# Performance work log

Hardware: AMD Instinct MI355X
Metric: run time of the kernel (lower is better)

## Reference

```python
import jax, jax.numpy as jnp
import numpy as np

INPUT_SIZE = 3072
CORE_SIZE = 1024
OUTPUT_SIZE = 100
BATCH = 8192


def _ri(key, shape, lo, hi):
    # small-range int8 values (torch rand*scale cast to int8)
    return jax.random.randint(key, shape, lo, hi, dtype=jnp.int32).astype(jnp.int8)


def setup_inputs() -> dict:
    key = jax.random.key(0)
    ks = jax.random.split(key, 14)
    return {
        # learned int8 weights (nonzero after EQI.apply updates)
        "W_itoc": _ri(ks[0], (INPUT_SIZE, CORE_SIZE), -3, 4),
        "W_itoc_b": _ri(ks[1], (CORE_SIZE,), -3, 4),
        "W_ctoc": _ri(ks[2], (CORE_SIZE, CORE_SIZE), -3, 4),
        "W_ctoc_b": _ri(ks[3], (CORE_SIZE,), -3, 4),
        "W_ctoo": _ri(ks[4], (CORE_SIZE, OUTPUT_SIZE), -3, 4),
        "W_ctoo_b": _ri(ks[5], (OUTPUT_SIZE,), -3, 4),
        # epsilon perturbations: EPSILON_SCALE=2 -> values in {-1,0,1}
        "e_itoc": _ri(ks[6], (INPUT_SIZE, CORE_SIZE), -2, 2),
        "e_itoc_b": _ri(ks[7], (CORE_SIZE,), -2, 2),
        "e_ctoc": _ri(ks[8], (CORE_SIZE, CORE_SIZE), -2, 2),
        "e_ctoc_b": _ri(ks[9], (CORE_SIZE,), -2, 2),
        "e_ctoo": _ri(ks[10], (CORE_SIZE, OUTPUT_SIZE), -2, 2),
        "e_ctoo_b": _ri(ks[11], (OUTPUT_SIZE,), -2, 2),
        # forward activations
        "inputs": _ri(ks[12], (BATCH, INPUT_SIZE), -4, 5),
        "hiddens": _ri(ks[13], (BATCH, CORE_SIZE), -4, 5),
    }


def _addmm_i8(x, w, b):
    # int8 addmm with wraparound semantics: accumulate in int32, cast back
    # to int8 (truncation == mod-256, matching torch int8 arithmetic).
    acc = jnp.matmul(x.astype(jnp.int32), w.astype(jnp.int32)) + b.astype(jnp.int32)
    return acc.astype(jnp.int8)


def reference(W_itoc, W_itoc_b, W_ctoc, W_ctoc_b, W_ctoo, W_ctoo_b,
              e_itoc, e_itoc_b, e_ctoc, e_ctoc_b, e_ctoo, e_ctoo_b,
              inputs, hiddens):
    # layer 1: inputs -> core (weight = W + epsilon, elementwise int8 add)
    i2c = _addmm_i8(inputs, W_itoc + e_itoc, W_itoc_b + e_itoc_b)      # [B, CORE]
    # layer 2: (hiddens + projected inputs) -> core
    h2 = _addmm_i8(hiddens + i2c, W_ctoc + e_ctoc, W_ctoc_b + e_ctoc_b)  # [B, CORE]
    # layer 3: core -> output
    out = _addmm_i8(h2, W_ctoo + e_ctoo, W_ctoo_b + e_ctoo_b)          # [B, OUT]
    return (h2, out)
```

## Files before the change

### kernel.cpp

```cpp
#include <hip/hip_runtime.h>

typedef int v4i  __attribute__((ext_vector_type(4)));
typedef int v16i __attribute__((ext_vector_type(16)));

__device__ __forceinline__ int pack4i(int a, int b, int c, int d) {
  return (a & 255) | ((b & 255) << 8) | ((c & 255) << 16) | ((d & 255) << 24);
}
__device__ __forceinline__ int badd4(int a, int b) {
  return ((a & 0x7f7f7f7f) + (b & 0x7f7f7f7f)) ^ ((a ^ b) & 0x80808080);
}

__device__ void pack_tile(const int* __restrict__ W, const int* __restrict__ E,
                          char* __restrict__ Bt, int K, int N,
                          int nx, int ky, char* lin) {
  const int t = threadIdx.x;
  const int n0 = nx * 64, k0 = ky * 256;
  {
    const int kk = t >> 2, c = t & 3;
    for (int p = 0; p < 4; ++p) {
      const int k = kk + (p << 6);
      const long grow = (long)(k0 + k) * N;
      #pragma unroll
      for (int i = 0; i < 4; ++i) {
        const int nl = (c << 4) + (i << 2);
        const int ng = n0 + nl;
        int a0, a1, a2, a3;
        if (ng + 3 < N) {
          int4 wv = *(const int4*)(W + grow + ng);
          int4 ev = *(const int4*)(E + grow + ng);
          a0 = wv.x + ev.x; a1 = wv.y + ev.y; a2 = wv.z + ev.z; a3 = wv.w + ev.w;
        } else {
          a0 = (ng + 0 < N) ? W[grow + ng + 0] + E[grow + ng + 0] : 0;
          a1 = (ng + 1 < N) ? W[grow + ng + 1] + E[grow + ng + 1] : 0;
          a2 = (ng + 2 < N) ? W[grow + ng + 2] + E[grow + ng + 2] : 0;
          a3 = (ng + 3 < N) ? W[grow + ng + 3] + E[grow + ng + 3] : 0;
        }
        *(int*)(lin + k * 68 + nl) = pack4i(a0, a1, a2, a3);
      }
    }
  }
  __syncthreads();
  {
    const int n = t & 63, kq = t >> 6;
    char* dst = Bt + (long)(n0 + n) * K + k0 + (kq << 6);
    int outv[16];
    #pragma unroll
    for (int g = 0; g < 16; ++g) {
      const int k = (kq << 6) + (g << 2);
      outv[g] = pack4i(lin[(k + 0) * 68 + n], lin[(k + 1) * 68 + n],
                       lin[(k + 2) * 68 + n], lin[(k + 3) * 68 + n]);
    }
    #pragma unroll
    for (int g = 0; g < 4; ++g)
      *(int4*)(dst + (g << 4)) =
          make_int4(outv[g * 4], outv[g * 4 + 1], outv[g * 4 + 2], outv[g * 4 + 3]);
  }
}

__device__ void pack_i32_to_i8(const int* __restrict__ src, char* __restrict__ dst,
                               long base, int iters) {
  const int t = threadIdx.x;
  for (int i = 0; i < iters; ++i) {
    const long i0 = base + ((long)(t + i * 256) << 4);
    const int* s = src + i0;
    int4 v0 = *(const int4*)(s);
    int4 v1 = *(const int4*)(s + 4);
    int4 v2 = *(const int4*)(s + 8);
    int4 v3 = *(const int4*)(s + 12);
    *(int4*)(dst + i0) = make_int4(
        pack4i(v0.x, v0.y, v0.z, v0.w), pack4i(v1.x, v1.y, v1.z, v1.w),
        pack4i(v2.x, v2.y, v2.z, v2.w), pack4i(v3.x, v3.y, v3.z, v3.w));
  }
}

__global__ __launch_bounds__(256) void pack_all_kernel(
    const int* W1, const int* E1, char* Bt1,
    const int* W2, const int* E2, char* Bt2,
    const int* W3, const int* E3, char* Bt3,
    const int* b1, const int* eb1, int* bs1,
    const int* b2, const int* eb2, int* bs2,
    const int* b3, const int* eb3, int* bs3,
    const int* X, char* X8, const int* H, char* H8) {
  __shared__ __align__(16) char lin[256 * 68];
  const int bid = blockIdx.x;
  if (bid < 192) {
    pack_tile(W1, E1, Bt1, 3072, 1024, bid % 16, bid / 16, lin);
  } else if (bid < 256) {
    const int l = bid - 192;
    pack_tile(W2, E2, Bt2, 1024, 1024, l % 16, l / 16, lin);
  } else if (bid < 264) {
    const int l = bid - 256;
    pack_tile(W3, E3, Bt3, 1024, 100, l & 1, l >> 1, lin);
  } else if (bid == 264) {
    const int t = threadIdx.x;
    for (int i = t; i < 1024; i += 256) {
      bs1[i] = b1[i] + eb1[i];
      bs2[i] = b2[i] + eb2[i];
    }
    for (int i = t; i < 128; i += 256)
      bs3[i] = (i < 100) ? (b3[i] + eb3[i]) : 0;
  } else if (bid < 1289) {
    pack_i32_to_i8(X, X8, (long)(bid - 265) * 24576, 6);
  } else {
    pack_i32_to_i8(H, H8, (long)(bid - 1289) * 32768, 8);
  }
}

template<int EPI>
__global__ __launch_bounds__(256, 4) void gemm_kernel(
    const char* __restrict__ A, const char* __restrict__ Btg,
    const int* __restrict__ bsum, const char* __restrict__ H8,
    char* __restrict__ A8out, int* __restrict__ Iout, const int K) {
  __shared__ __align__(16) char smem[30720];

  const int t = threadIdx.x;
  const int bid = blockIdx.x;
  const int mt = bid & 127, nt = bid >> 7;
  const long m0 = (long)mt << 6;
  const int n0 = nt << 7;

  const int lane = t & 63, w = t >> 6;
  const int lc = lane & 31, hg = lane >> 5;

  v16i acc[2] = {};

  const int am = t >> 2, ah = t & 3;
  const char* Arow = A + (m0 + am) * (long)K + ah * 16;
  const int aoff = am * 80 + ah * 16;
  const int bm = t >> 1, bh = t & 1;
  const char* Brow = Btg + (long)(n0 + bm) * K + bh * 32;
  const int boff = bm * 80 + bh * 32;

  const int abo = lc * 80 + hg * 16;
  const int bbo = (w * 32 + lc) * 80 + hg * 16;

  int4 ar, br0, br1;
  auto LOAD = [&](int kb) {
    ar  = *(const int4*)(Arow + kb);
    br0 = *(const int4*)(Brow + kb);
    br1 = *(const int4*)(Brow + kb + 16);
  };
  auto STORE = [&](int stage) {
    char* base = smem + stage * 15360;
    *(int4*)(base + aoff) = ar;
    *(int4*)(base + 5120 + boff)      = br0;
    *(int4*)(base + 5120 + boff + 16) = br1;
  };

  const int kiters = K >> 6;
  LOAD(0);
  STORE(0);
  __syncthreads();

  for (int kt = 0; kt < kiters; ++kt) {
    if (kt + 1 < kiters) LOAD((kt + 1) << 6);
    const char* base = smem + (kt & 1) * 15360;
    const char* Ab = base + abo;
    const char* Bb = base + 5120 + bbo;
    #pragma unroll
    for (int ks = 0; ks < 2; ++ks) {
      v4i a0 = *(const v4i*)(Ab + ks * 32);
      v4i a1 = *(const v4i*)(Ab + 32 * 80 + ks * 32);
      v4i b  = *(const v4i*)(Bb + ks * 32);
      acc[0] = __builtin_amdgcn_mfma_i32_32x32x32_i8(a0, b, acc[0], 0, 0, 0);
      acc[1] = __builtin_amdgcn_mfma_i32_32x32x32_i8(a1, b, acc[1], 0, 0, 0);
    }
    if (kt + 1 < kiters) {
      STORE((kt + 1) & 1);
      __syncthreads();
    }
  }

  const int gcl = w * 32 + lc;
  const int bs = bsum[n0 + gcl];
  if (EPI == 1) {
    #pragma unroll
    for (int tm = 0; tm < 2; ++tm) {
      #pragma unroll
      for (int r = 0; r < 16; ++r) {
        const int row = tm * 32 + (hg << 2) + (r & 3) + ((r >> 2) << 3);
        Iout[(m0 + row) * 1024 + n0 + gcl] = (int)(signed char)(acc[tm][r] + bs);
      }
    }
  } else {
    __syncthreads();
    #pragma unroll
    for (int tm = 0; tm < 2; ++tm) {
      #pragma unroll
      for (int r = 0; r < 16; ++r) {
        const int row = tm * 32 + (hg << 2) + (r & 3) + ((r >> 2) << 3);
        smem[row * 144 + gcl] = (char)(acc[tm][r] + bs);
      }
    }
    __syncthreads();
    const char* src = smem + (t >> 2) * 144 + (t & 3) * 32;
    const long gm = m0 + (t >> 2);
    const long gco = gm * 1024 + n0 + (t & 3) * 32;
    int4 s0 = *(const int4*)(src);
    int4 s1 = *(const int4*)(src + 16);
    int4 h0 = *(const int4*)(H8 + gco);
    int4 h1 = *(const int4*)(H8 + gco + 16);
    s0 = make_int4(badd4(s0.x, h0.x), badd4(s0.y, h0.y),
                   badd4(s0.z, h0.z), badd4(s0.w, h0.w));
    s1 = make_int4(badd4(s1.x, h1.x), badd4(s1.y, h1.y),
                   badd4(s1.z, h1.z), badd4(s1.w, h1.w));
    *(int4*)(A8out + gco)      = s0;
    *(int4*)(A8out + gco + 16) = s1;
  }
}

__global__ __launch_bounds__(256, 2) void gemm3_kernel(
    const int* __restrict__ h2, const char* __restrict__ Btg,
    const int* __restrict__ bsum, int* __restrict__ Iout) {
  __shared__ __align__(16) char smem[25600];
  const int t = threadIdx.x;
  const int m0 = blockIdx.x << 5;
  const int lane = t & 63, w = t >> 6;
  const int lc = lane & 31, hg = lane >> 5;
  v16i acc = {};

  const int am = t >> 3, ah = t & 7;
  const long arow = (long)(m0 + am) * 1024 + ah * 8;
  const int aoff = am * 80 + ah * 8;
  const int bm = t >> 1, bh = t & 1;
  const char* Brow = Btg + (long)bm * 1024 + bh * 32;
  const int boff = bm * 80 + bh * 32;

  int4 ar[2]; int4 br[2];
  auto LOAD = [&](int kb) {
    const int* Ar = h2 + arow + kb;
    ar[0] = *(const int4*)(Ar);
    ar[1] = *(const int4*)(Ar + 4);
    br[0] = *(const int4*)(Brow + kb);
    br[1] = *(const int4*)(Brow + kb + 16);
  };
  auto STORE = [&](int stage) {
    char* As_ = smem + stage * 12800;
    char* Bs_ = As_ + 2560;
    int2 d;
    d.x = pack4i(ar[0].x, ar[0].y, ar[0].z, ar[0].w);
    d.y = pack4i(ar[1].x, ar[1].y, ar[1].z, ar[1].w);
    *(int2*)(As_ + aoff) = d;
    *(int4*)(Bs_ + boff)      = br[0];
    *(int4*)(Bs_ + boff + 16) = br[1];
  };

  LOAD(0); STORE(0); __syncthreads();
  for (int kt = 0; kt < 16; ++kt) {
    if (kt + 1 < 16) LOAD((kt + 1) << 6);
    const char* base = smem + (kt & 1) * 12800;
    const char* Ab = base + lc * 80 + hg * 16;
    const char* Bb = base + 2560 + (w * 32 + lc) * 80 + hg * 16;
    #pragma unroll
    for (int ks = 0; ks < 2; ++ks) {
      v4i a = *(const v4i*)(Ab + ks * 32);
      v4i b = *(const v4i*)(Bb + ks * 32);
      acc = __builtin_amdgcn_mfma_i32_32x32x32_i8(a, b, acc, 0, 0, 0);
    }
    if (kt + 1 < 16) { STORE((kt + 1) & 1); __syncthreads(); }
  }

  const int gcl = w * 32 + lc;
  if (gcl < 100) {
    const int bs = bsum[gcl];
    #pragma unroll
    for (int r = 0; r < 16; ++r) {
      const int row = (r & 3) + ((r >> 2) << 3) + (hg << 2);
      Iout[(long)(m0 + row) * 100 + gcl] = (int)(signed char)(acc[r] + bs);
    }
  }
}

extern "C" void kernel_launch(void* const* d_in, const int* in_sizes, int n_in,
                              void* d_out, int out_size, void* d_ws, size_t ws_size,
                              hipStream_t stream) {
  (void)in_sizes; (void)n_in; (void)out_size; (void)ws_size;
  const int* W1  = (const int*)d_in[0];
  const int* b1  = (const int*)d_in[1];
  const int* W2  = (const int*)d_in[2];
  const int* b2  = (const int*)d_in[3];
  const int* W3  = (const int*)d_in[4];
  const int* b3  = (const int*)d_in[5];
  const int* E1  = (const int*)d_in[6];
  const int* eb1 = (const int*)d_in[7];
  const int* E2  = (const int*)d_in[8];
  const int* eb2 = (const int*)d_in[9];
  const int* E3  = (const int*)d_in[10];
  const int* eb3 = (const int*)d_in[11];
  const int* X   = (const int*)d_in[12];
  const int* H   = (const int*)d_in[13];
  int* out = (int*)d_out;

  char* ws  = (char*)d_ws;
  char* Bt1 = ws;
  char* Bt2 = Bt1 + 3145728;
  char* Bt3 = Bt2 + 1048576;
  int*  bs1 = (int*)(Bt3 + 131072);
  int*  bs2 = bs1 + 1024;
  int*  bs3 = bs2 + 1024;
  char* A2  = (char*)(bs3 + 128);
  char* X8  = (char*)d_out;
  char* H8  = X8 + 25165824;

  pack_all_kernel<<<dim3(1545), dim3(256), 0, stream>>>(
      W1, E1, Bt1, W2, E2, Bt2, W3, E3, Bt3,
      b1, eb1, bs1, b2, eb2, bs2, b3, eb3, bs3, X, X8, H, H8);

  gemm_kernel<0><<<dim3(1024), dim3(256), 0, stream>>>(
      X8, Bt1, bs1, H8, A2, nullptr, 3072);

  gemm_kernel<1><<<dim3(1024), dim3(256), 0, stream>>>(
      A2, Bt2, bs2, nullptr, nullptr, out, 1024);

  gemm3_kernel<<<dim3(256), dim3(256), 0, stream>>>(
      out, Bt3, bs3, out + 8388608);
}
```

Measured before the change: 315.2 us.

## Deepen register prefetch in GEMM loops and batch loads in int8 packing

The GEMM main loops are unrolled by two and now hold two register sets, so global loads for tiles k+2 and k+3 are issued while MFMAs run on the current shared-memory stage. This gives memory latency more time to hide behind compute. The int32-to-int8 packing routine now issues G groups of loads before doing any packing or stores, which raises memory-level parallelism. The cost is higher register pressure, which could lower occupancy under the launch bounds.

```diff
diff --git a/kernel.cpp b/kernel.cpp
--- a/kernel.cpp
+++ b/kernel.cpp
@@ -57,19 +57,30 @@
   }
 }
 
-__device__ void pack_i32_to_i8(const int* __restrict__ src, char* __restrict__ dst,
-                               long base, int iters) {
+template<int G>
+__device__ void pack_ilp(const int* __restrict__ src, char* __restrict__ dst,
+                         long base, int supers) {
   const int t = threadIdx.x;
-  for (int i = 0; i < iters; ++i) {
-    const long i0 = base + ((long)(t + i * 256) << 4);
-    const int* s = src + i0;
-    int4 v0 = *(const int4*)(s);
-    int4 v1 = *(const int4*)(s + 4);
-    int4 v2 = *(const int4*)(s + 8);
-    int4 v3 = *(const int4*)(s + 12);
-    *(int4*)(dst + i0) = make_int4(
-        pack4i(v0.x, v0.y, v0.z, v0.w), pack4i(v1.x, v1.y, v1.z, v1.w),
-        pack4i(v2.x, v2.y, v2.z, v2.w), pack4i(v3.x, v3.y, v3.z, v3.w));
+  for (int s = 0; s < supers; ++s) {
+    int4 v[G][4];
+    #pragma unroll
+    for (int g = 0; g < G; ++g) {
+      const long i0 = base + ((long)(t + (s * G + g) * 256) << 4);
+      const int* p = src + i0;
+      v[g][0] = ((const int4*)p)[0];
+      v[g][1] = ((const int4*)p)[1];
+      v[g][2] = ((const int4*)p)[2];
+      v[g][3] = ((const int4*)p)[3];
+    }
+    #pragma unroll
+    for (int g = 0; g < G; ++g) {
+      const long i0 = base + ((long)(t + (s * G + g) * 256) << 4);
+      *(int4*)(dst + i0) = make_int4(
+          pack4i(v[g][0].x, v[g][0].y, v[g][0].z, v[g][0].w),
+          pack4i(v[g][1].x, v[g][1].y, v[g][1].z, v[g][1].w),
+          pack4i(v[g][2].x, v[g][2].y, v[g][2].z, v[g][2].w),
+          pack4i(v[g][3].x, v[g][3].y, v[g][3].z, v[g][3].w));
+    }
   }
 }
 
@@ -100,9 +111,9 @@
     for (int i = t; i < 128; i += 256)
       bs3[i] = (i < 100) ? (b3[i] + eb3[i]) : 0;
   } else if (bid < 1289) {
-    pack_i32_to_i8(X, X8, (long)(bid - 265) * 24576, 6);
+    pack_ilp<3>(X, X8, (long)(bid - 265) * 24576, 2);
   } else {
-    pack_i32_to_i8(H, H8, (long)(bid - 1289) * 32768, 8);
+    pack_ilp<4>(H, H8, (long)(bid - 1289) * 32768, 2);
   }
 }
 
@@ -134,27 +145,22 @@
   const int abo = lc * 80 + hg * 16;
   const int bbo = (w * 32 + lc) * 80 + hg * 16;
 
-  int4 ar, br0, br1;
-  auto LOAD = [&](int kb) {
-    ar  = *(const int4*)(Arow + kb);
-    br0 = *(const int4*)(Brow + kb);
-    br1 = *(const int4*)(Brow + kb + 16);
-  };
-  auto STORE = [&](int stage) {
+  int4 a0r, b0r0, b0r1;
+  int4 a1r, b1r0, b1r1;
+
+  auto LOAD = [&](int kb, int4& a, int4& b0, int4& b1) {
+    a  = *(const int4*)(Arow + kb);
+    b0 = *(const int4*)(Brow + kb);
+    b1 = *(const int4*)(Brow + kb + 16);
+  };
+  auto STORE = [&](int stage, const int4& a, const int4& b0, const int4& b1) {
     char* base = smem + stage * 15360;
-    *(int4*)(base + aoff) = ar;
-    *(int4*)(base + 5120 + boff)      = br0;
-    *(int4*)(base + 5120 + boff + 16) = br1;
-  };
-
-  const int kiters = K >> 6;
-  LOAD(0);
-  STORE(0);
-  __syncthreads();
-
-  for (int kt = 0; kt < kiters; ++kt) {
-    if (kt + 1 < kiters) LOAD((kt + 1) << 6);
-    const char* base = smem + (kt & 1) * 15360;
+    *(int4*)(base + aoff) = a;
+    *(int4*)(base + 5120 + boff)      = b0;
+    *(int4*)(base + 5120 + boff + 16) = b1;
+  };
+  auto MFMA = [&](int stage) {
+    const char* base = smem + stage * 15360;
     const char* Ab = base + abo;
     const char* Bb = base + 5120 + bbo;
     #pragma unroll
@@ -165,8 +171,23 @@
       acc[0] = __builtin_amdgcn_mfma_i32_32x32x32_i8(a0, b, acc[0], 0, 0, 0);
       acc[1] = __builtin_amdgcn_mfma_i32_32x32x32_i8(a1, b, acc[1], 0, 0, 0);
     }
-    if (kt + 1 < kiters) {
-      STORE((kt + 1) & 1);
+  };
+
+  const int kiters = K >> 6;
+  LOAD(0, a0r, b0r0, b0r1);
+  STORE(0, a0r, b0r0, b0r1);
+  LOAD(64, a1r, b1r0, b1r1);
+  __syncthreads();
+
+  for (int kt = 0; kt < kiters; kt += 2) {
+    MFMA(0);
+    if (kt + 2 < kiters) LOAD((kt + 2) << 6, a0r, b0r0, b0r1);
+    STORE(1, a1r, b1r0, b1r1);
+    __syncthreads();
+    MFMA(1);
+    if (kt + 3 < kiters) LOAD((kt + 3) << 6, a1r, b1r0, b1r1);
+    if (kt + 2 < kiters) {
+      STORE(0, a0r, b0r0, b0r1);
       __syncthreads();
     }
   }
@@ -226,29 +247,29 @@
   const char* Brow = Btg + (long)bm * 1024 + bh * 32;
   const int boff = bm * 80 + bh * 32;
 
-  int4 ar[2]; int4 br[2];
-  auto LOAD = [&](int kb) {
+  int4 a0r0, a0r1, b0r0, b0r1;
+  int4 a1r0, a1r1, b1r0, b1r1;
+
+  auto LOAD = [&](int kb, int4& a0, int4& a1, int4& b0, int4& b1) {
     const int* Ar = h2 + arow + kb;
-    ar[0] = *(const int4*)(Ar);
-    ar[1] = *(const int4*)(Ar + 4);
-    br[0] = *(const int4*)(Brow + kb);
-    br[1] = *(const int4*)(Brow + kb + 16);
-  };
-  auto STORE = [&](int stage) {
+    a0 = *(const int4*)(Ar);
+    a1 = *(const int4*)(Ar + 4);
+    b0 = *(const int4*)(Brow + kb);
+    b1 = *(const int4*)(Brow + kb + 16);
+  };
+  auto STORE = [&](int stage, const int4& a0, const int4& a1,
+                   const int4& b0, const int4& b1) {
     char* As_ = smem + stage * 12800;
     char* Bs_ = As_ + 2560;
     int2 d;
-    d.x = pack4i(ar[0].x, ar[0].y, ar[0].z, ar[0].w);
-    d.y = pack4i(ar[1].x, ar[1].y, ar[1].z, ar[1].w);
+    d.x = pack4i(a0.x, a0.y, a0.z, a0.w);
+    d.y = pack4i(a1.x, a1.y, a1.z, a1.w);
     *(int2*)(As_ + aoff) = d;
-    *(int4*)(Bs_ + boff)      = br[0];
-    *(int4*)(Bs_ + boff + 16) = br[1];
-  };
-
-  LOAD(0); STORE(0); __syncthreads();
-  for (int kt = 0; kt < 16; ++kt) {
-    if (kt + 1 < 16) LOAD((kt + 1) << 6);
-    const char* base = smem + (kt & 1) * 12800;
+    *(int4*)(Bs_ + boff)      = b0;
+    *(int4*)(Bs_ + boff + 16) = b1;
+  };
+  auto MFMA = [&](int stage) {
+    const char* base = smem + stage * 12800;
     const char* Ab = base + lc * 80 + hg * 16;
     const char* Bb = base + 2560 + (w * 32 + lc) * 80 + hg * 16;
     #pragma unroll
@@ -257,7 +278,24 @@
       v4i b = *(const v4i*)(Bb + ks * 32);
       acc = __builtin_amdgcn_mfma_i32_32x32x32_i8(a, b, acc, 0, 0, 0);
     }
-    if (kt + 1 < 16) { STORE((kt + 1) & 1); __syncthreads(); }
+  };
+
+  LOAD(0, a0r0, a0r1, b0r0, b0r1);
+  STORE(0, a0r0, a0r1, b0r0, b0r1);
+  LOAD(64, a1r0, a1r1, b1r0, b1r1);
+  __syncthreads();
+
+  for (int kt = 0; kt < 16; kt += 2) {
+    MFMA(0);
+    if (kt + 2 < 16) LOAD((kt + 2) << 6, a0r0, a0r1, b0r0, b0r1);
+    STORE(1, a1r0, a1r1, b1r0, b1r1);
+    __syncthreads();
+    MFMA(1);
+    if (kt + 3 < 16) LOAD((kt + 3) << 6, a1r0, a1r1, b1r0, b1r1);
+    if (kt + 2 < 16) {
+      STORE(0, a0r0, a0r1, b0r0, b0r1);
+      __syncthreads();
+    }
   }
 
   const int gcl = w * 32 + lc;
```

Measured after the change: 321.7 us. 1.02x slower.

## Fuse int32-to-int8 activation packing into GEMM loads; retile final GEMM

Applied to the files above, without the earlier changes.

Drops the separate pass that converted the int32 X and H activations to int8. The first GEMM now reads int32 X directly and packs it to int8 when staging into shared memory, and its epilogue reads int32 H directly. This removes one write and one re-read of the int8 copies. In exchange, layer 1 reads its A operand as int32 on every N-tile block, which is 4x the bytes per load and repeated across the 8 N tiles. The third GEMM moves to 16x16x64 MFMA with 16-row tiles and twice as many blocks, to spread it across more compute units.

```diff
diff --git a/kernel.cpp b/kernel.cpp
--- a/kernel.cpp
+++ b/kernel.cpp
@@ -57,30 +57,13 @@
   }
 }
 
-__device__ void pack_i32_to_i8(const int* __restrict__ src, char* __restrict__ dst,
-                               long base, int iters) {
-  const int t = threadIdx.x;
-  for (int i = 0; i < iters; ++i) {
-    const long i0 = base + ((long)(t + i * 256) << 4);
-    const int* s = src + i0;
-    int4 v0 = *(const int4*)(s);
-    int4 v1 = *(const int4*)(s + 4);
-    int4 v2 = *(const int4*)(s + 8);
-    int4 v3 = *(const int4*)(s + 12);
-    *(int4*)(dst + i0) = make_int4(
-        pack4i(v0.x, v0.y, v0.z, v0.w), pack4i(v1.x, v1.y, v1.z, v1.w),
-        pack4i(v2.x, v2.y, v2.z, v2.w), pack4i(v3.x, v3.y, v3.z, v3.w));
-  }
-}
-
 __global__ __launch_bounds__(256) void pack_all_kernel(
     const int* W1, const int* E1, char* Bt1,
     const int* W2, const int* E2, char* Bt2,
     const int* W3, const int* E3, char* Bt3,
     const int* b1, const int* eb1, int* bs1,
     const int* b2, const int* eb2, int* bs2,
-    const int* b3, const int* eb3, int* bs3,
-    const int* X, char* X8, const int* H, char* H8) {
+    const int* b3, const int* eb3, int* bs3) {
   __shared__ __align__(16) char lin[256 * 68];
   const int bid = blockIdx.x;
   if (bid < 192) {
@@ -91,7 +74,7 @@
   } else if (bid < 264) {
     const int l = bid - 256;
     pack_tile(W3, E3, Bt3, 1024, 100, l & 1, l >> 1, lin);
-  } else if (bid == 264) {
+  } else {
     const int t = threadIdx.x;
     for (int i = t; i < 1024; i += 256) {
       bs1[i] = b1[i] + eb1[i];
@@ -99,17 +82,13 @@
     }
     for (int i = t; i < 128; i += 256)
       bs3[i] = (i < 100) ? (b3[i] + eb3[i]) : 0;
-  } else if (bid < 1289) {
-    pack_i32_to_i8(X, X8, (long)(bid - 265) * 24576, 6);
-  } else {
-    pack_i32_to_i8(H, H8, (long)(bid - 1289) * 32768, 8);
-  }
-}
-
-template<int EPI>
+  }
+}
+
+template<int MODE>
 __global__ __launch_bounds__(256, 4) void gemm_kernel(
-    const char* __restrict__ A, const char* __restrict__ Btg,
-    const int* __restrict__ bsum, const char* __restrict__ H8,
+    const void* __restrict__ Asrc, const char* __restrict__ Btg,
+    const int* __restrict__ bsum, const int* __restrict__ H,
     char* __restrict__ A8out, int* __restrict__ Iout, const int K) {
   __shared__ __align__(16) char smem[30720];
 
@@ -125,8 +104,9 @@
   v16i acc[2] = {};
 
   const int am = t >> 2, ah = t & 3;
-  const char* Arow = A + (m0 + am) * (long)K + ah * 16;
   const int aoff = am * 80 + ah * 16;
+  const int*  Arow32 = (const int*)Asrc + (m0 + am) * (long)K + ah * 16;
+  const char* Arow8  = (const char*)Asrc + (m0 + am) * (long)K + ah * 16;
   const int bm = t >> 1, bh = t & 1;
   const char* Brow = Btg + (long)(n0 + bm) * K + bh * 32;
   const int boff = bm * 80 + bh * 32;
@@ -134,27 +114,37 @@
   const int abo = lc * 80 + hg * 16;
   const int bbo = (w * 32 + lc) * 80 + hg * 16;
 
-  int4 ar, br0, br1;
-  auto LOAD = [&](int kb) {
-    ar  = *(const int4*)(Arow + kb);
+  int4 ar[4], br0, br1;
+  auto LOAD = [&](int kt) {
+    const int kb = kt << 6;
+    if (MODE == 1) {
+      const int* p = Arow32 + kb;
+      ar[0] = ((const int4*)p)[0];
+      ar[1] = ((const int4*)p)[1];
+      ar[2] = ((const int4*)p)[2];
+      ar[3] = ((const int4*)p)[3];
+    } else {
+      ar[0] = *(const int4*)(Arow8 + kb);
+    }
     br0 = *(const int4*)(Brow + kb);
     br1 = *(const int4*)(Brow + kb + 16);
   };
   auto STORE = [&](int stage) {
     char* base = smem + stage * 15360;
-    *(int4*)(base + aoff) = ar;
+    if (MODE == 1) {
+      *(int4*)(base + aoff) = make_int4(
+          pack4i(ar[0].x, ar[0].y, ar[0].z, ar[0].w),
+          pack4i(ar[1].x, ar[1].y, ar[1].z, ar[1].w),
+          pack4i(ar[2].x, ar[2].y, ar[2].z, ar[2].w),
+          pack4i(ar[3].x, ar[3].y, ar[3].z, ar[3].w));
+    } else {
+      *(int4*)(base + aoff) = ar[0];
+    }
     *(int4*)(base + 5120 + boff)      = br0;
     *(int4*)(base + 5120 + boff + 16) = br1;
   };
-
-  const int kiters = K >> 6;
-  LOAD(0);
-  STORE(0);
-  __syncthreads();
-
-  for (int kt = 0; kt < kiters; ++kt) {
-    if (kt + 1 < kiters) LOAD((kt + 1) << 6);
-    const char* base = smem + (kt & 1) * 15360;
+  auto MFMA = [&](int stage) {
+    const char* base = smem + stage * 15360;
     const char* Ab = base + abo;
     const char* Bb = base + 5120 + bbo;
     #pragma unroll
@@ -165,6 +155,16 @@
       acc[0] = __builtin_amdgcn_mfma_i32_32x32x32_i8(a0, b, acc[0], 0, 0, 0);
       acc[1] = __builtin_amdgcn_mfma_i32_32x32x32_i8(a1, b, acc[1], 0, 0, 0);
     }
+  };
+
+  const int kiters = K >> 6;
+  LOAD(0);
+  STORE(0);
+  __syncthreads();
+
+  for (int kt = 0; kt < kiters; ++kt) {
+    if (kt + 1 < kiters) LOAD(kt + 1);
+    MFMA(kt & 1);
     if (kt + 1 < kiters) {
       STORE((kt + 1) & 1);
       __syncthreads();
@@ -173,7 +173,7 @@
 
   const int gcl = w * 32 + lc;
   const int bs = bsum[n0 + gcl];
-  if (EPI == 1) {
+  if (MODE == 2) {
     #pragma unroll
     for (int tm = 0; tm < 2; ++tm) {
       #pragma unroll
@@ -193,17 +193,24 @@
       }
     }
     __syncthreads();
-    const char* src = smem + (t >> 2) * 144 + (t & 3) * 32;
-    const long gm = m0 + (t >> 2);
-    const long gco = gm * 1024 + n0 + (t & 3) * 32;
+    const int rr = t >> 2, rc = (t & 3) * 32;
+    const char* src = smem + rr * 144 + rc;
+    const long gco = (m0 + rr) * 1024 + n0 + rc;
     int4 s0 = *(const int4*)(src);
     int4 s1 = *(const int4*)(src + 16);
-    int4 h0 = *(const int4*)(H8 + gco);
-    int4 h1 = *(const int4*)(H8 + gco + 16);
-    s0 = make_int4(badd4(s0.x, h0.x), badd4(s0.y, h0.y),
-                   badd4(s0.z, h0.z), badd4(s0.w, h0.w));
-    s1 = make_int4(badd4(s1.x, h1.x), badd4(s1.y, h1.y),
-                   badd4(s1.z, h1.z), badd4(s1.w, h1.w));
+    const int* Hp = H + gco;
+    int4 h0 = ((const int4*)Hp)[0], h1 = ((const int4*)Hp)[1];
+    int4 h2v = ((const int4*)Hp)[2], h3 = ((const int4*)Hp)[3];
+    int4 h4 = ((const int4*)Hp)[4], h5 = ((const int4*)Hp)[5];
+    int4 h6 = ((const int4*)Hp)[6], h7 = ((const int4*)Hp)[7];
+    s0.x = badd4(s0.x, pack4i(h0.x, h0.y, h0.z, h0.w));
+    s0.y = badd4(s0.y, pack4i(h1.x, h1.y, h1.z, h1.w));
+    s0.z = badd4(s0.z, pack4i(h2v.x, h2v.y, h2v.z, h2v.w));
+    s0.w = badd4(s0.w, pack4i(h3.x, h3.y, h3.z, h3.w));
+    s1.x = badd4(s1.x, pack4i(h4.x, h4.y, h4.z, h4.w));
+    s1.y = badd4(s1.y, pack4i(h5.x, h5.y, h5.z, h5.w));
+    s1.z = badd4(s1.z, pack4i(h6.x, h6.y, h6.z, h6.w));
+    s1.w = badd4(s1.w, pack4i(h7.x, h7.y, h7.z, h7.w));
     *(int4*)(A8out + gco)      = s0;
     *(int4*)(A8out + gco + 16) = s1;
   }
@@ -212,62 +219,66 @@
 __global__ __launch_bounds__(256, 2) void gemm3_kernel(
     const int* __restrict__ h2, const char* __restrict__ Btg,
     const int* __restrict__ bsum, int* __restrict__ Iout) {
-  __shared__ __align__(16) char smem[25600];
+  __shared__ __align__(16) char smem[23040];
   const int t = threadIdx.x;
-  const int m0 = blockIdx.x << 5;
+  const int m0 = blockIdx.x << 4;
   const int lane = t & 63, w = t >> 6;
-  const int lc = lane & 31, hg = lane >> 5;
-  v16i acc = {};
-
-  const int am = t >> 3, ah = t & 7;
-  const long arow = (long)(m0 + am) * 1024 + ah * 8;
-  const int aoff = am * 80 + ah * 8;
+  const int l16 = lane & 15, q = lane >> 4;
+  v4i acc0 = {}, acc1 = {};
+
+  const int am = t >> 4, ah = t & 15;
+  const int* Arow = h2 + (long)(m0 + am) * 1024 + ah * 4;
+  const int aoff = am * 80 + ah * 4;
   const int bm = t >> 1, bh = t & 1;
   const char* Brow = Btg + (long)bm * 1024 + bh * 32;
   const int boff = bm * 80 + bh * 32;
 
-  int4 ar[2]; int4 br[2];
-  auto LOAD = [&](int kb) {
-    const int* Ar = h2 + arow + kb;
-    ar[0] = *(const int4*)(Ar);
-    ar[1] = *(const int4*)(Ar + 4);
-    br[0] = *(const int4*)(Brow + kb);
-    br[1] = *(const int4*)(Brow + kb + 16);
+  const int abo  = l16 * 80 + q * 16;
+  const int bbo0 = (w * 32 + l16) * 80 + q * 16;
+  const int bbo1 = (w * 32 + 16 + l16) * 80 + q * 16;
+
+  int4 ar, br0, br1;
+  auto LOAD = [&](int kt) {
+    const int kb = kt << 6;
+    ar  = *(const int4*)(Arow + kb);
+    br0 = *(const int4*)(Brow + kb);
+    br1 = *(const int4*)(Brow + kb + 16);
   };
   auto STORE = [&](int stage) {
-    char* As_ = smem + stage * 12800;
-    char* Bs_ = As_ + 2560;
-    int2 d;
-    d.x = pack4i(ar[0].x, ar[0].y, ar[0].z, ar[0].w);
-    d.y = pack4i(ar[1].x, ar[1].y, ar[1].z, ar[1].w);
-    *(int2*)(As_ + aoff) = d;
-    *(int4*)(Bs_ + boff)      = br[0];
-    *(int4*)(Bs_ + boff + 16) = br[1];
+    char* base = smem + stage * 11520;
+    *(int*)(base + aoff) = pack4i(ar.x, ar.y, ar.z, ar.w);
+    *(int4*)(base + 1280 + boff)      = br0;
+    *(int4*)(base + 1280 + boff + 16) = br1;
+  };
+  auto MFMA = [&](int stage) {
+    const char* base = smem + stage * 11520;
+    v4i a  = *(const v4i*)(base + abo);
+    v4i b0 = *(const v4i*)(base + 1280 + bbo0);
+    v4i b1 = *(const v4i*)(base + 1280 + bbo1);
+    acc0 = __builtin_amdgcn_mfma_i32_16x16x64_i8(a, b0, acc0, 0, 0, 0);
+    acc1 = __builtin_amdgcn_mfma_i32_16x16x64_i8(a, b1, acc1, 0, 0, 0);
   };
 
   LOAD(0); STORE(0); __syncthreads();
   for (int kt = 0; kt < 16; ++kt) {
-    if (kt + 1 < 16) LOAD((kt + 1) << 6);
-    const char* base = smem + (kt & 1) * 12800;
-    const char* Ab = base + lc * 80 + hg * 16;
-    const char* Bb = base + 2560 + (w * 32 + lc) * 80 + hg * 16;
-    #pragma unroll
-    for (int ks = 0; ks < 2; ++ks) {
-      v4i a = *(const v4i*)(Ab + ks * 32);
-      v4i b = *(const v4i*)(Bb + ks * 32);
-      acc = __builtin_amdgcn_mfma_i32_32x32x32_i8(a, b, acc, 0, 0, 0);
-    }
+    if (kt + 1 < 16) LOAD(kt + 1);
+    MFMA(kt & 1);
     if (kt + 1 < 16) { STORE((kt + 1) & 1); __syncthreads(); }
   }
 
-  const int gcl = w * 32 + lc;
-  if (gcl < 100) {
-    const int bs = bsum[gcl];
-    #pragma unroll
-    for (int r = 0; r < 16; ++r) {
-      const int row = (r & 3) + ((r >> 2) << 3) + (hg << 2);
-      Iout[(long)(m0 + row) * 100 + gcl] = (int)(signed char)(acc[r] + bs);
-    }
+  const int c0 = w * 32 + l16;
+  const int c1 = c0 + 16;
+  if (c0 < 100) {
+    const int b = bsum[c0];
+    #pragma unroll
+    for (int r = 0; r < 4; ++r)
+      Iout[(long)(m0 + q * 4 + r) * 100 + c0] = (int)(signed char)(acc0[r] + b);
+  }
+  if (c1 < 100) {
+    const int b = bsum[c1];
+    #pragma unroll
+    for (int r = 0; r < 4; ++r)
+      Iout[(long)(m0 + q * 4 + r) * 100 + c1] = (int)(signed char)(acc1[r] + b);
   }
 }
 
@@ -299,19 +310,17 @@
   int*  bs2 = bs1 + 1024;
   int*  bs3 = bs2 + 1024;
   char* A2  = (char*)(bs3 + 128);
-  char* X8  = (char*)d_out;
-  char* H8  = X8 + 25165824;
-
-  pack_all_kernel<<<dim3(1545), dim3(256), 0, stream>>>(
+
+  pack_all_kernel<<<dim3(265), dim3(256), 0, stream>>>(
       W1, E1, Bt1, W2, E2, Bt2, W3, E3, Bt3,
-      b1, eb1, bs1, b2, eb2, bs2, b3, eb3, bs3, X, X8, H, H8);
-
-  gemm_kernel<0><<<dim3(1024), dim3(256), 0, stream>>>(
-      X8, Bt1, bs1, H8, A2, nullptr, 3072);
+      b1, eb1, bs1, b2, eb2, bs2, b3, eb3, bs3);
 
   gemm_kernel<1><<<dim3(1024), dim3(256), 0, stream>>>(
+      X, Bt1, bs1, H, A2, nullptr, 3072);
+
+  gemm_kernel<2><<<dim3(1024), dim3(256), 0, stream>>>(
       A2, Bt2, bs2, nullptr, nullptr, out, 1024);
 
-  gemm3_kernel<<<dim3(256), dim3(256), 0, stream>>>(
+  gemm3_kernel<<<dim3(512), dim3(256), 0, stream>>>(
       out, Bt3, bs3, out + 8388608);
 }
```

After: 350.9 us. 1.11x slower.
